# Optimization experiments

Hardware: AMD Instinct MI355X
Metric: run time of the kernel (lower is better)

## Reference

```python
import jax, jax.numpy as jnp
import numpy as np

EMBED_DIM = 1024
N_HEAD = 16

def setup_inputs() -> dict:
    key = jax.random.key(0)
    ks = jax.random.split(key, 5)
    C = EMBED_DIM
    x = jax.random.normal(ks[0], (2, 2048, C), dtype=jnp.float32)
    s = 1.0 / np.sqrt(C)
    W_attn = jax.random.normal(ks[1], (C, 3 * C), dtype=jnp.float32) * s
    b_attn = jnp.zeros((3 * C,), dtype=jnp.float32)
    W_proj = jax.random.normal(ks[2], (C, C), dtype=jnp.float32) * s
    b_proj = jnp.zeros((C,), dtype=jnp.float32)
    return {"x": x, "W_attn": W_attn, "b_attn": b_attn, "W_proj": W_proj, "b_proj": b_proj}

def reference(x, W_attn, b_attn, W_proj, b_proj):
    B, T, C = x.shape
    H = N_HEAD
    D = C // H
    qkv = x @ W_attn + b_attn                      # [B,T,3C]
    q, k, v = jnp.split(qkv, 3, axis=-1)
    # [B,H,T,D]
    q = q.reshape(B, T, H, D).transpose(0, 2, 1, 3)
    k = k.reshape(B, T, H, D).transpose(0, 2, 1, 3)
    v = v.reshape(B, T, H, D).transpose(0, 2, 1, 3)
    att = jnp.einsum('bhqd,bhkd->bhqk', q, k) * (1.0 / jnp.sqrt(jnp.asarray(D, x.dtype)))
    causal = jnp.tril(jnp.ones((T, T), dtype=bool))
    att = jnp.where(causal, att, -jnp.inf)
    att = jax.nn.softmax(att, axis=-1)
    y = jnp.einsum('bhqk,bhkd->bhqd', att, v)      # [B,H,T,D]
    y = y.transpose(0, 2, 1, 3).reshape(B, T, C)
    return y @ W_proj + b_proj
```

## Files before the change

### kernel.cpp

```cpp
#include <hip/hip_runtime.h>
#include <stdint.h>

typedef __attribute__((ext_vector_type(4))) float f32x4;
typedef __attribute__((ext_vector_type(8))) __bf16 bf16x8;
typedef __attribute__((ext_vector_type(8))) unsigned short u16x8;
typedef __attribute__((ext_vector_type(4))) unsigned short u16x4;

__device__ __forceinline__ unsigned short f2b(float f) {
  unsigned u = __float_as_uint(f);
  u += 0x7FFFu + ((u >> 16) & 1u);
  return (unsigned short)(u >> 16);
}
__device__ __forceinline__ float b2f(unsigned short s) {
  unsigned u = (unsigned)s << 16;
  return __uint_as_float(u);
}
__device__ __forceinline__ unsigned cvtpk_bf16(float lo, float hi) {
  unsigned r;
  asm("v_cvt_pk_bf16_f32 %0, %1, %2" : "=v"(r) : "v"(lo), "v"(hi));
  return r;
}

__device__ __forceinline__ void gload_lds16(const void* g, void* l) {
  typedef __attribute__((address_space(1))) void GV1;
  typedef __attribute__((address_space(3))) void LV3;
  __builtin_amdgcn_global_load_lds((GV1*)(void*)g, (LV3*)l, 16, 0, 0);
}

__global__ __launch_bounds__(256) void convert_f32_bf16(const float* __restrict__ in,
                                                        unsigned short* __restrict__ out, int n) {
  int i = (blockIdx.x * 256 + threadIdx.x) * 8;
  if (i >= n) return;
  float4 a = *(const float4*)(in + i);
  float4 b = *(const float4*)(in + i + 4);
  u16x8 r;
  r[0] = f2b(a.x); r[1] = f2b(a.y); r[2] = f2b(a.z); r[3] = f2b(a.w);
  r[4] = f2b(b.x); r[5] = f2b(b.y); r[6] = f2b(b.z); r[7] = f2b(b.w);
  *(u16x8*)(out + i) = r;
}

__global__ __launch_bounds__(256) void transpose_f32_bf16(const float* __restrict__ W,
                                                          unsigned short* __restrict__ Wt,
                                                          int K, int N) {
  __shared__ unsigned short tile[32][33];
  int n0 = blockIdx.x * 32, k0 = blockIdx.y * 32;
  int tx = threadIdx.x, ty = threadIdx.y;
  #pragma unroll
  for (int j = 0; j < 32; j += 8)
    tile[ty + j][tx] = f2b(W[(size_t)(k0 + ty + j) * N + n0 + tx]);
  __syncthreads();
  #pragma unroll
  for (int j = 0; j < 32; j += 8)
    Wt[(size_t)(n0 + ty + j) * K + k0 + tx] = tile[tx][ty + j];
}

template <bool OUT_BF16>
__global__ __launch_bounds__(256) void gemm_bt(const unsigned short* __restrict__ A,
                                               const unsigned short* __restrict__ Bt,
                                               const float* __restrict__ bias,
                                               void* __restrict__ Cout,
                                               int M, int N, int K) {
  __shared__ unsigned short As[128 * 64];
  __shared__ unsigned short Bs[128 * 64];
  const int m0 = blockIdx.x * 128, n0 = blockIdx.y * 128;
  const int tid = threadIdx.x;
  const int w = tid >> 6, l = tid & 63;
  const int wm = w >> 1, wn = w & 1;
  const int c = l & 15, g = l >> 4;
  f32x4 acc[4][4] = {};
  for (int k0 = 0; k0 < K; k0 += 64) {
    #pragma unroll
    for (int i = 0; i < 4; ++i) {
      int rb = w * 32 + i * 8;
      gload_lds16(A + (size_t)(m0 + rb + (l >> 3)) * K + k0 + (l & 7) * 8, &As[rb * 64]);
      gload_lds16(Bt + (size_t)(n0 + rb + (l >> 3)) * K + k0 + (l & 7) * 8, &Bs[rb * 64]);
    }
    __syncthreads();
    #pragma unroll
    for (int ks = 0; ks < 2; ++ks) {
      bf16x8 af[4], bf[4];
      #pragma unroll
      for (int mi = 0; mi < 4; ++mi)
        af[mi] = *(const bf16x8*)&As[(wm * 64 + mi * 16 + c) * 64 + ks * 32 + g * 8];
      #pragma unroll
      for (int ni = 0; ni < 4; ++ni)
        bf[ni] = *(const bf16x8*)&Bs[(wn * 64 + ni * 16 + c) * 64 + ks * 32 + g * 8];
      #pragma unroll
      for (int mi = 0; mi < 4; ++mi)
        #pragma unroll
        for (int ni = 0; ni < 4; ++ni)
          acc[mi][ni] = __builtin_amdgcn_mfma_f32_16x16x32_bf16(af[mi], bf[ni], acc[mi][ni], 0, 0, 0);
    }
    __syncthreads();
  }
  #pragma unroll
  for (int mi = 0; mi < 4; ++mi) {
    #pragma unroll
    for (int ni = 0; ni < 4; ++ni) {
      int colg = n0 + wn * 64 + ni * 16 + c;
      float bv = bias[colg];
      #pragma unroll
      for (int r = 0; r < 4; ++r) {
        int rowg = m0 + wm * 64 + mi * 16 + 4 * g + r;
        float v = acc[mi][ni][r] + bv;
        if (OUT_BF16)
          ((unsigned short*)Cout)[(size_t)rowg * N + colg] = f2b(v);
        else
          ((float*)Cout)[(size_t)rowg * N + colg] = v;
      }
    }
  }
}

__global__ __launch_bounds__(512) void attn_kernel(const unsigned short* __restrict__ qkv,
                                                   unsigned short* __restrict__ partO,
                                                   float* __restrict__ partML) {
  __shared__ unsigned short K_lds[2][64 * 64];
  __shared__ unsigned short V_lds[2][64 * 64];
  const int bid = blockIdx.x;
  const int bh = bid & 31;
  const int cid = 39 - (bid >> 5);
  int qt, ct;
  if (cid < 4)       { qt = cid;            ct = 0; }
  else if (cid < 12) { int e = cid - 4;  qt = 4 + (e >> 1);  ct = e & 1; }
  else if (cid < 24) { int e = cid - 12; int q3 = e / 3; qt = 8 + q3; ct = e - 3 * q3; }
  else               { int e = cid - 24; qt = 12 + (e >> 2); ct = e & 3; }
  const int ntt = 2 * qt + 2;
  const int t0 = ct * 8;
  const int ntl = min(ntt - t0, 8);
  const int b = bh >> 4, h = bh & 15;
  const int tid = threadIdx.x, w = tid >> 6, l = tid & 63;
  const int c = l & 15, g = l >> 4;
  const int hi = g >> 1;
  const int srcA = c + ((g & 1) << 5);
  const int srcB = srcA + 16;
  const size_t row0 = (size_t)b * 2048;
  const int vp = tid & 31, vcb = tid >> 5;
  const float SCL = 0.18033688f;
  const int TSTRIDE = 64 * 3072;

  const int q0w = qt * 128 + w * 16;
  const int qg = q0w + c;

  bf16x8 qf[2];
  #pragma unroll
  for (int ks = 0; ks < 2; ++ks)
    qf[ks] = *(const bf16x8*)(qkv + (row0 + qg) * 3072 + h * 64 + ks * 32 + g * 8);

  f32x4 acc[4] = {};
  float mstate = -1e30f, lstate = 0.f;

  const int krow = w * 8 + (l >> 3);
  const int kch = (l & 7) ^ (krow & 7);
  const unsigned short* kptr = qkv + (row0 + t0 * 64 + krow) * 3072 + 1024 + h * 64 + kch * 8;
  const unsigned short* vptr = qkv + (row0 + t0 * 64 + 2 * vp) * 3072 + 2048 + h * 64 + vcb * 4;
  const int kdst = (w * 8) * 64;
  int voff[4];
  #pragma unroll
  for (int jj = 0; jj < 4; ++jj) {
    int d = vcb * 4 + jj;
    voff[jj] = d * 128 + ((4 * vp) ^ ((d & 7) << 4));
  }

  {
    gload_lds16(kptr, &K_lds[0][kdst]);
    u16x4 v0 = *(const u16x4*)vptr;
    u16x4 v1 = *(const u16x4*)(vptr + 3072);
    char* Vb = (char*)V_lds[0];
    #pragma unroll
    for (int jj = 0; jj < 4; ++jj)
      *(unsigned int*)(Vb + voff[jj]) = (unsigned int)v0[jj] | ((unsigned int)v1[jj] << 16);
  }
  __syncthreads();

  for (int lt = 0; lt < ntl; ++lt) {
    const int cur = lt & 1;
    const int kv0 = (t0 + lt) * 64;
    const bool pre = (lt + 1 < ntl);
    u16x4 v0n, v1n;
    if (pre) {
      gload_lds16(kptr + TSTRIDE, &K_lds[cur ^ 1][kdst]);
      v0n = *(const u16x4*)(vptr + TSTRIDE);
      v1n = *(const u16x4*)(vptr + TSTRIDE + 3072);
    }
    kptr += TSTRIDE;
    vptr += TSTRIDE;
    if (kv0 <= q0w + 15) {
      const char* Kb = (const char*)K_lds[cur];
      const char* Vb = (const char*)V_lds[cur];
      f32x4 s[4] = {};
      #pragma unroll
      for (int ks = 0; ks < 2; ++ks) {
        bf16x8 kf[4];
        #pragma unroll
        for (int nk = 0; nk < 4; ++nk) {
          int row = nk * 16 + c;
          kf[nk] = *(const bf16x8*)(Kb + row * 128 + ((ks * 64 + g * 16) ^ ((row & 7) << 4)));
        }
        __builtin_amdgcn_s_setprio(1);
        #pragma unroll
        for (int nk = 0; nk < 4; ++nk)
          s[nk] = __builtin_amdgcn_mfma_f32_16x16x32_bf16(kf[nk], qf[ks], s[nk], 0, 0, 0);
        __builtin_amdgcn_s_setprio(0);
      }
      if (kv0 + 63 > q0w) {
        #pragma unroll
        for (int nk = 0; nk < 4; ++nk)
          #pragma unroll
          for (int r = 0; r < 4; ++r) {
            int kvg = kv0 + nk * 16 + 4 * g + r;
            if (kvg > qg) s[nk][r] = -1e30f;
          }
      }
      float a0 = fmaxf(fmaxf(s[0][0], s[0][1]), fmaxf(s[0][2], s[0][3]));
      float a1 = fmaxf(fmaxf(s[1][0], s[1][1]), fmaxf(s[1][2], s[1][3]));
      float a2 = fmaxf(fmaxf(s[2][0], s[2][1]), fmaxf(s[2][2], s[2][3]));
      float a3 = fmaxf(fmaxf(s[3][0], s[3][1]), fmaxf(s[3][2], s[3][3]));
      float mx = fmaxf(fmaxf(a0, a1), fmaxf(a2, a3));
      mx = fmaxf(mx, __shfl_xor(mx, 16));
      mx = fmaxf(mx, __shfl_xor(mx, 32));
      if (!__all(mx <= mstate)) {
        float mnew = fmaxf(mstate, mx);
        float alpha = exp2f((mstate - mnew) * SCL);
        mstate = mnew;
        lstate *= alpha;
        #pragma unroll
        for (int nd = 0; nd < 4; ++nd) acc[nd] *= alpha;
      }
      float ms = mstate * SCL;
      #pragma unroll
      for (int nk = 0; nk < 4; ++nk) {
        #pragma unroll
        for (int r = 0; r < 4; ++r) s[nk][r] = exp2f(fmaf(s[nk][r], SCL, -ms));
        lstate += (s[nk][0] + s[nk][1]) + (s[nk][2] + s[nk][3]);
      }
      unsigned pk[4][2];
      #pragma unroll
      for (int nk = 0; nk < 4; ++nk) {
        pk[nk][0] = cvtpk_bf16(s[nk][0], s[nk][1]);
        pk[nk][1] = cvtpk_bf16(s[nk][2], s[nk][3]);
      }
      #pragma unroll
      for (int vks = 0; vks < 2; ++vks) {
        unsigned rA00 = __shfl(pk[2 * vks][0], srcA, 64);
        unsigned rA01 = __shfl(pk[2 * vks][1], srcA, 64);
        unsigned rA10 = __shfl(pk[2 * vks + 1][0], srcA, 64);
        unsigned rA11 = __shfl(pk[2 * vks + 1][1], srcA, 64);
        unsigned rB00 = __shfl(pk[2 * vks][0], srcB, 64);
        unsigned rB01 = __shfl(pk[2 * vks][1], srcB, 64);
        unsigned rB10 = __shfl(pk[2 * vks + 1][0], srcB, 64);
        unsigned rB11 = __shfl(pk[2 * vks + 1][1], srcB, 64);
        union { unsigned u[4]; bf16x8 v; } pa;
        pa.u[0] = hi ? rA10 : rA00;
        pa.u[1] = hi ? rA11 : rA01;
        pa.u[2] = hi ? rB10 : rB00;
        pa.u[3] = hi ? rB11 : rB01;
        bf16x8 vf[4];
        #pragma unroll
        for (int nd = 0; nd < 4; ++nd) {
          int row = nd * 16 + c;
          vf[nd] = *(const bf16x8*)(Vb + row * 128 + ((vks * 64 + g * 16) ^ ((row & 7) << 4)));
        }
        __builtin_amdgcn_s_setprio(1);
        #pragma unroll
        for (int nd = 0; nd < 4; ++nd)
          acc[nd] = __builtin_amdgcn_mfma_f32_16x16x32_bf16(vf[nd], pa.v, acc[nd], 0, 0, 0);
        __builtin_amdgcn_s_setprio(0);
      }
    }
    if (pre) {
      char* Vbn = (char*)V_lds[cur ^ 1];
      #pragma unroll
      for (int jj = 0; jj < 4; ++jj)
        *(unsigned int*)(Vbn + voff[jj]) = (unsigned int)v0n[jj] | ((unsigned int)v1n[jj] << 16);
    }
    __syncthreads();
  }

  float lsum = lstate;
  lsum += __shfl_xor(lsum, 16);
  lsum += __shfl_xor(lsum, 32);
  const int qrow = w * 16 + c;
  #pragma unroll
  for (int nd = 0; nd < 4; ++nd) {
    ushort4 o4;
    o4.x = f2b(acc[nd][0]); o4.y = f2b(acc[nd][1]);
    o4.z = f2b(acc[nd][2]); o4.w = f2b(acc[nd][3]);
    *(ushort4*)(partO + (size_t)bid * 8192 + qrow * 64 + nd * 16 + 4 * g) = o4;
  }
  if (g == 0) {
    partML[(size_t)bid * 256 + qrow * 2 + 0] = mstate;
    partML[(size_t)bid * 256 + qrow * 2 + 1] = lsum;
  }
}

__global__ __launch_bounds__(256) void attn_combine(const unsigned short* __restrict__ partO,
                                                    const float* __restrict__ partML,
                                                    unsigned short* __restrict__ out) {
  const int bid = blockIdx.x;
  const int qt = bid >> 5, bh = bid & 31;
  const int b = bh >> 4, h = bh & 15;
  const int np = (2 * qt + 9) >> 3;
  const int base = (qt < 4) ? qt
                 : (qt < 8) ? 4 + 2 * (qt - 4)
                 : (qt < 12) ? 12 + 3 * (qt - 8)
                 : 24 + 4 * (qt - 12);
  const int t = threadIdx.x;
  const int row = t >> 1, cg = (t & 1) * 32;
  const float SCL = 0.18033688f;
  float mstar = -1e30f;
  #pragma unroll
  for (int p = 0; p < 4; ++p)
    if (p < np)
      mstar = fmaxf(mstar, partML[(size_t)(((39 - (base + p)) << 5) | bh) * 256 + row * 2]);
  float L = 0.f;
  float o[32];
  #pragma unroll
  for (int j = 0; j < 32; ++j) o[j] = 0.f;
  #pragma unroll
  for (int p = 0; p < 4; ++p) {
    if (p < np) {
      int slot = ((39 - (base + p)) << 5) | bh;
      float mp = partML[(size_t)slot * 256 + row * 2 + 0];
      float lp = partML[(size_t)slot * 256 + row * 2 + 1];
      float wgt = exp2f((mp - mstar) * SCL);
      L = fmaf(wgt, lp, L);
      const unsigned short* src = partO + (size_t)slot * 8192 + row * 64 + cg;
      #pragma unroll
      for (int q = 0; q < 4; ++q) {
        u16x8 a = *(const u16x8*)(src + q * 8);
        #pragma unroll
        for (int j = 0; j < 8; ++j)
          o[q * 8 + j] = fmaf(b2f(a[j]), wgt, o[q * 8 + j]);
      }
    }
  }
  float rinv = 1.0f / L;
  size_t trow = (size_t)b * 2048 + qt * 128 + row;
  #pragma unroll
  for (int q = 0; q < 4; ++q) {
    u16x8 r;
    #pragma unroll
    for (int j = 0; j < 8; ++j) r[j] = f2b(o[q * 8 + j] * rinv);
    *(u16x8*)(out + trow * 1024 + h * 64 + cg + q * 8) = r;
  }
}

extern "C" void kernel_launch(void* const* d_in, const int* in_sizes, int n_in,
                              void* d_out, int out_size, void* d_ws, size_t ws_size,
                              hipStream_t stream) {
  const float* x      = (const float*)d_in[0];
  const float* W_attn = (const float*)d_in[1];
  const float* b_attn = (const float*)d_in[2];
  const float* W_proj = (const float*)d_in[3];
  const float* b_proj = (const float*)d_in[4];
  float* out = (float*)d_out;

  char* ws = (char*)d_ws;
  unsigned short* Wproj_t  = (unsigned short*)(ws + 0);
  unsigned short* qkv      = (unsigned short*)(ws + 2097152);
  unsigned short* x_bf     = (unsigned short*)(ws + 27262976);
  unsigned short* Wattn_t  = (unsigned short*)(ws + 35651584);
  unsigned short* partO    = (unsigned short*)(ws + 27262976);
  unsigned short* attn_out = (unsigned short*)(ws + 48234496);
  float*          partML   = (float*)(ws + 56623104);

  convert_f32_bf16<<<2048, 256, 0, stream>>>(x, x_bf, 4194304);
  transpose_f32_bf16<<<dim3(96, 32), dim3(32, 8), 0, stream>>>(W_attn, Wattn_t, 1024, 3072);
  transpose_f32_bf16<<<dim3(32, 32), dim3(32, 8), 0, stream>>>(W_proj, Wproj_t, 1024, 1024);

  gemm_bt<true><<<dim3(32, 24), 256, 0, stream>>>(x_bf, Wattn_t, b_attn, qkv, 4096, 3072, 1024);
  attn_kernel<<<1280, 512, 0, stream>>>(qkv, partO, partML);
  attn_combine<<<512, 256, 0, stream>>>(partO, partML, attn_out);
  gemm_bt<false><<<dim3(32, 8), 256, 0, stream>>>(attn_out, Wproj_t, b_proj, out, 4096, 1024, 1024);
}
```

Before: 150.9 us.

## Emit V transposed from QKV GEMM epilogue and async-load it in attention

The QKV GEMM now writes Q/K to a narrower [T,2048] buffer and writes V transposed ([C,T]) through an LDS-staged epilogue. The attention kernel can then fill V tiles with the same direct global-to-LDS 16-byte loads used for K, instead of register loads plus packed, swizzled LDS stores after each compute step. This removes VGPR staging and extra LDS writes from the attention inner loop. In exchange the GEMM epilogue for V blocks gains an LDS transpose and a sync, and the V tile layout in LDS must still match the swizzle the PV reads expect.

```diff
diff --git a/kernel.cpp b/kernel.cpp
--- a/kernel.cpp
+++ b/kernel.cpp
@@ -4,7 +4,6 @@
 typedef __attribute__((ext_vector_type(4))) float f32x4;
 typedef __attribute__((ext_vector_type(8))) __bf16 bf16x8;
 typedef __attribute__((ext_vector_type(8))) unsigned short u16x8;
-typedef __attribute__((ext_vector_type(4))) unsigned short u16x4;
 
 __device__ __forceinline__ unsigned short f2b(float f) {
   unsigned u = __float_as_uint(f);
@@ -54,14 +53,16 @@
     Wt[(size_t)(n0 + ty + j) * K + k0 + tx] = tile[tx][ty + j];
 }
 
-template <bool OUT_BF16>
+template <bool OUT_BF16, bool VSPLIT>
 __global__ __launch_bounds__(256) void gemm_bt(const unsigned short* __restrict__ A,
                                                const unsigned short* __restrict__ Bt,
                                                const float* __restrict__ bias,
                                                void* __restrict__ Cout,
+                                               unsigned short* __restrict__ vT,
                                                int M, int N, int K) {
-  __shared__ unsigned short As[128 * 64];
-  __shared__ unsigned short Bs[128 * 64];
+  __shared__ unsigned short SMEM[128 * 136];
+  unsigned short* As = SMEM;
+  unsigned short* Bs = SMEM + 8192;
   const int m0 = blockIdx.x * 128, n0 = blockIdx.y * 128;
   const int tid = threadIdx.x;
   const int w = tid >> 6, l = tid & 63;
@@ -93,6 +94,30 @@
     }
     __syncthreads();
   }
+  if (VSPLIT && n0 >= 2048) {
+    #pragma unroll
+    for (int mi = 0; mi < 4; ++mi)
+      #pragma unroll
+      for (int ni = 0; ni < 4; ++ni) {
+        int cl = wn * 64 + ni * 16 + c;
+        float bv = bias[n0 + cl];
+        #pragma unroll
+        for (int r = 0; r < 4; ++r) {
+          int rl = wm * 64 + mi * 16 + 4 * g + r;
+          SMEM[cl * 136 + rl] = f2b(acc[mi][ni][r] + bv);
+        }
+      }
+    __syncthreads();
+    const int d0 = n0 - 2048;
+    #pragma unroll
+    for (int p = 0; p < 8; ++p) {
+      int rowl = p * 16 + (tid >> 4);
+      *(u16x8*)(vT + (size_t)(d0 + rowl) * 4096 + m0 + (tid & 15) * 8) =
+          *(const u16x8*)&SMEM[rowl * 136 + (tid & 15) * 8];
+    }
+    return;
+  }
+  const int NS = VSPLIT ? 2048 : N;
   #pragma unroll
   for (int mi = 0; mi < 4; ++mi) {
     #pragma unroll
@@ -104,15 +129,16 @@
         int rowg = m0 + wm * 64 + mi * 16 + 4 * g + r;
         float v = acc[mi][ni][r] + bv;
         if (OUT_BF16)
-          ((unsigned short*)Cout)[(size_t)rowg * N + colg] = f2b(v);
+          ((unsigned short*)Cout)[(size_t)rowg * NS + colg] = f2b(v);
         else
-          ((float*)Cout)[(size_t)rowg * N + colg] = v;
-      }
-    }
-  }
-}
-
-__global__ __launch_bounds__(512) void attn_kernel(const unsigned short* __restrict__ qkv,
+          ((float*)Cout)[(size_t)rowg * NS + colg] = v;
+      }
+    }
+  }
+}
+
+__global__ __launch_bounds__(512) void attn_kernel(const unsigned short* __restrict__ qk,
+                                                   const unsigned short* __restrict__ vT,
                                                    unsigned short* __restrict__ partO,
                                                    float* __restrict__ partML) {
   __shared__ unsigned short K_lds[2][64 * 64];
@@ -135,9 +161,9 @@
   const int srcA = c + ((g & 1) << 5);
   const int srcB = srcA + 16;
   const size_t row0 = (size_t)b * 2048;
-  const int vp = tid & 31, vcb = tid >> 5;
   const float SCL = 0.18033688f;
-  const int TSTRIDE = 64 * 3072;
+  const int KSTRIDE = 64 * 2048;
+  const int VSTRIDE = 64;
 
   const int q0w = qt * 128 + w * 16;
   const int qg = q0w + c;
@@ -145,46 +171,31 @@
   bf16x8 qf[2];
   #pragma unroll
   for (int ks = 0; ks < 2; ++ks)
-    qf[ks] = *(const bf16x8*)(qkv + (row0 + qg) * 3072 + h * 64 + ks * 32 + g * 8);
+    qf[ks] = *(const bf16x8*)(qk + (row0 + qg) * 2048 + h * 64 + ks * 32 + g * 8);
 
   f32x4 acc[4] = {};
   float mstate = -1e30f, lstate = 0.f;
 
   const int krow = w * 8 + (l >> 3);
   const int kch = (l & 7) ^ (krow & 7);
-  const unsigned short* kptr = qkv + (row0 + t0 * 64 + krow) * 3072 + 1024 + h * 64 + kch * 8;
-  const unsigned short* vptr = qkv + (row0 + t0 * 64 + 2 * vp) * 3072 + 2048 + h * 64 + vcb * 4;
+  const unsigned short* kptr = qk + (row0 + t0 * 64 + krow) * 2048 + 1024 + h * 64 + kch * 8;
+  const unsigned short* vptr = vT + (size_t)(h * 64 + krow) * 4096 + (b * 2048 + t0 * 64) + kch * 8;
   const int kdst = (w * 8) * 64;
-  int voff[4];
-  #pragma unroll
-  for (int jj = 0; jj < 4; ++jj) {
-    int d = vcb * 4 + jj;
-    voff[jj] = d * 128 + ((4 * vp) ^ ((d & 7) << 4));
-  }
-
-  {
-    gload_lds16(kptr, &K_lds[0][kdst]);
-    u16x4 v0 = *(const u16x4*)vptr;
-    u16x4 v1 = *(const u16x4*)(vptr + 3072);
-    char* Vb = (char*)V_lds[0];
-    #pragma unroll
-    for (int jj = 0; jj < 4; ++jj)
-      *(unsigned int*)(Vb + voff[jj]) = (unsigned int)v0[jj] | ((unsigned int)v1[jj] << 16);
-  }
+
+  gload_lds16(kptr, &K_lds[0][kdst]);
+  gload_lds16(vptr, &V_lds[0][kdst]);
   __syncthreads();
 
   for (int lt = 0; lt < ntl; ++lt) {
     const int cur = lt & 1;
     const int kv0 = (t0 + lt) * 64;
     const bool pre = (lt + 1 < ntl);
-    u16x4 v0n, v1n;
     if (pre) {
-      gload_lds16(kptr + TSTRIDE, &K_lds[cur ^ 1][kdst]);
-      v0n = *(const u16x4*)(vptr + TSTRIDE);
-      v1n = *(const u16x4*)(vptr + TSTRIDE + 3072);
-    }
-    kptr += TSTRIDE;
-    vptr += TSTRIDE;
+      gload_lds16(kptr + KSTRIDE, &K_lds[cur ^ 1][kdst]);
+      gload_lds16(vptr + VSTRIDE, &V_lds[cur ^ 1][kdst]);
+    }
+    kptr += KSTRIDE;
+    vptr += VSTRIDE;
     if (kv0 <= q0w + 15) {
       const char* Kb = (const char*)K_lds[cur];
       const char* Vb = (const char*)V_lds[cur];
@@ -268,12 +279,6 @@
         __builtin_amdgcn_s_setprio(0);
       }
     }
-    if (pre) {
-      char* Vbn = (char*)V_lds[cur ^ 1];
-      #pragma unroll
-      for (int jj = 0; jj < 4; ++jj)
-        *(unsigned int*)(Vbn + voff[jj]) = (unsigned int)v0n[jj] | ((unsigned int)v1n[jj] << 16);
-    }
     __syncthreads();
   }
 
@@ -358,7 +363,8 @@
 
   char* ws = (char*)d_ws;
   unsigned short* Wproj_t  = (unsigned short*)(ws + 0);
-  unsigned short* qkv      = (unsigned short*)(ws + 2097152);
+  unsigned short* qk       = (unsigned short*)(ws + 2097152);
+  unsigned short* vT       = (unsigned short*)(ws + 18874368);
   unsigned short* x_bf     = (unsigned short*)(ws + 27262976);
   unsigned short* Wattn_t  = (unsigned short*)(ws + 35651584);
   unsigned short* partO    = (unsigned short*)(ws + 27262976);
@@ -369,8 +375,10 @@
   transpose_f32_bf16<<<dim3(96, 32), dim3(32, 8), 0, stream>>>(W_attn, Wattn_t, 1024, 3072);
   transpose_f32_bf16<<<dim3(32, 32), dim3(32, 8), 0, stream>>>(W_proj, Wproj_t, 1024, 1024);
 
-  gemm_bt<true><<<dim3(32, 24), 256, 0, stream>>>(x_bf, Wattn_t, b_attn, qkv, 4096, 3072, 1024);
-  attn_kernel<<<1280, 512, 0, stream>>>(qkv, partO, partML);
+  gemm_bt<true, true><<<dim3(32, 24), 256, 0, stream>>>(x_bf, Wattn_t, b_attn, qk, vT,
+                                                        4096, 3072, 1024);
+  attn_kernel<<<1280, 512, 0, stream>>>(qk, vT, partO, partML);
   attn_combine<<<512, 256, 0, stream>>>(partO, partML, attn_out);
-  gemm_bt<false><<<dim3(32, 8), 256, 0, stream>>>(attn_out, Wproj_t, b_proj, out, 4096, 1024, 1024);
-}
+  gemm_bt<false, false><<<dim3(32, 8), 256, 0, stream>>>(attn_out, Wproj_t, b_proj, out, nullptr,
+                                                         4096, 1024, 1024);
+}
```

After: 148.4 us. No clear change (-1.7%).
